# Kernel tuning notes

Measured on AMD Instinct MI355X. Metric: run time of the kernel, lower is better.

## Reference

```python
import jax, jax.numpy as jnp
import numpy as np

DIM = 768
HEADS = 12
HEAD_DIM = DIM // HEADS


def setup_inputs() -> dict:
    key = jax.random.key(0)
    ks = jax.random.split(key, 5)
    s = 0.02
    return {
        "x": jax.random.normal(ks[0], (2, 4096, DIM), dtype=jnp.float32),
        "w_qkv": jax.random.normal(ks[1], (DIM, 3 * DIM), dtype=jnp.float32) * s,
        "b_qkv": jax.random.normal(ks[2], (3 * DIM,), dtype=jnp.float32) * s,
        "w_proj": jax.random.normal(ks[3], (DIM, DIM), dtype=jnp.float32) * s,
        "b_proj": jax.random.normal(ks[4], (DIM,), dtype=jnp.float32) * s,
    }


def reference(x, w_qkv, b_qkv, w_proj, b_proj):
    B, N, _ = x.shape
    scale = HEAD_DIM ** (-0.5)
    qkv = x @ w_qkv + b_qkv                              # [B, N, 3*DIM]
    q, k, v = jnp.split(qkv, 3, axis=-1)
    # 'b n (h d) -> b h n d'
    def to_heads(t):
        return t.reshape(B, N, HEADS, HEAD_DIM).transpose(0, 2, 1, 3)
    q, k, v = to_heads(q), to_heads(k), to_heads(v)
    attn = jnp.einsum('bhnd,bhmd->bhnm', q, k) * scale   # [B, H, N, N]
    attn = jax.nn.softmax(attn, axis=-1)
    out = jnp.einsum('bhnm,bhmd->bhnd', attn, v)         # [B, H, N, D]
    out = out.transpose(0, 2, 1, 3).reshape(B, N, DIM)   # 'b h n d -> b n (h d)'
    return out @ w_proj + b_proj
```

## Files before the change

### kernel.cpp

```cpp
#include <hip/hip_runtime.h>
#include <hip/hip_bf16.h>
#include <stdint.h>

typedef _Float16 f16x8 __attribute__((ext_vector_type(8)));
typedef _Float16 f16x4 __attribute__((ext_vector_type(4)));
typedef uint32_t u32x2 __attribute__((ext_vector_type(2)));
typedef float floatx4 __attribute__((ext_vector_type(4)));

#define NSEQ 4096
#define DIMM 768
#define NHEADS 12
#define HD 64

__device__ __forceinline__ void gload_lds16(const void* g, void* l) {
  typedef __attribute__((address_space(1))) const uint32_t GQ;
  typedef __attribute__((address_space(3))) uint32_t LQ;
  __builtin_amdgcn_global_load_lds((GQ*)g, (LQ*)l, 16, 0, 0);
}

__device__ __forceinline__ uint16_t f16_bits(float v) {
  _Float16 h = (_Float16)v;
  return __builtin_bit_cast(uint16_t, h);
}

__device__ __forceinline__ uint32_t pkrtz(float a, float b) {
  return __builtin_bit_cast(uint32_t, __builtin_amdgcn_cvt_pkrtz(a, b));
}

__device__ __forceinline__ int swz(int row, int e) {
  return row * 64 + ((((e >> 3) ^ (row & 7)) << 3) | (e & 7));
}

__global__ __launch_bounds__(256) void convert_f32_f16(
    const float4* __restrict__ src, f16x8* __restrict__ dst, int n8) {
  const int i = blockIdx.x * 256 + threadIdx.x;
  if (i >= n8) return;
  const float4 a = src[2 * i], b = src[2 * i + 1];
  f16x8 o;
  o[0] = (_Float16)a.x; o[1] = (_Float16)a.y; o[2] = (_Float16)a.z; o[3] = (_Float16)a.w;
  o[4] = (_Float16)b.x; o[5] = (_Float16)b.y; o[6] = (_Float16)b.z; o[7] = (_Float16)b.w;
  dst[i] = o;
}

__global__ __launch_bounds__(256) void transpose_f32_f16(
    const float* __restrict__ src, uint16_t* __restrict__ dst, int R, int C) {
  __shared__ uint16_t tile[32][33];
  const int c0 = blockIdx.x * 32, r0 = blockIdx.y * 32;
  const int tx = threadIdx.x, ty = threadIdx.y;
#pragma unroll
  for (int i = 0; i < 32; i += 8)
    tile[ty + i][tx] = f16_bits(src[(size_t)(r0 + ty + i) * C + (c0 + tx)]);
  __syncthreads();
#pragma unroll
  for (int i = 0; i < 32; i += 8)
    dst[(size_t)(c0 + ty + i) * R + (r0 + tx)] = tile[tx][ty + i];
}

__global__ __launch_bounds__(256) void transpose_b16(
    const uint16_t* __restrict__ src, uint16_t* __restrict__ dst, int R, int C) {
  __shared__ uint16_t tile[32][33];
  const size_t plane = (size_t)blockIdx.z * (size_t)R * (size_t)C;
  const int c0 = blockIdx.x * 32, r0 = blockIdx.y * 32;
  const int tx = threadIdx.x, ty = threadIdx.y;
#pragma unroll
  for (int i = 0; i < 32; i += 8)
    tile[ty + i][tx] = src[plane + (size_t)(r0 + ty + i) * C + (c0 + tx)];
  __syncthreads();
#pragma unroll
  for (int i = 0; i < 32; i += 8)
    dst[plane + (size_t)(c0 + ty + i) * R + (r0 + tx)] = tile[tx][ty + i];
}

__global__ __launch_bounds__(256) void gemm_bt(
    const _Float16* __restrict__ A, const _Float16* __restrict__ Bt,
    const float* __restrict__ bias, int K, int mode,
    void* __restrict__ o0, _Float16* __restrict__ o1, _Float16* __restrict__ o2) {
  __shared__ __attribute__((aligned(16))) _Float16 As[128 * 32];
  __shared__ __attribute__((aligned(16))) _Float16 Bs[128 * 32];
  __shared__ float bias_s[128];
  const int tid = threadIdx.x;
  const int wv = tid >> 6;
  const int lane = tid & 63;
  const int quad = lane >> 4, l16 = lane & 15;
  const int wm = (wv >> 1) * 64, wn = (wv & 1) * 64;
  const int m0 = blockIdx.y * 128, n0 = blockIdx.x * 128;

  if (tid < 128) bias_s[tid] = bias[n0 + tid];

  floatx4 acc[4][4];
#pragma unroll
  for (int i = 0; i < 4; ++i)
#pragma unroll
    for (int j = 0; j < 4; ++j) acc[i][j] = (floatx4){0.f, 0.f, 0.f, 0.f};

  const int ar = tid >> 2, ac = (tid & 3) * 8;
  const _Float16* A0 = A + (size_t)(m0 + ar) * K + ac;
  const _Float16* A1 = A + (size_t)(m0 + 64 + ar) * K + ac;
  const _Float16* B0 = Bt + (size_t)(n0 + ar) * K + ac;
  const _Float16* B1 = Bt + (size_t)(n0 + 64 + ar) * K + ac;

  for (int kt = 0; kt < K; kt += 32) {
    const f16x8 ra0 = *(const f16x8*)(A0 + kt);
    const f16x8 ra1 = *(const f16x8*)(A1 + kt);
    const f16x8 rb0 = *(const f16x8*)(B0 + kt);
    const f16x8 rb1 = *(const f16x8*)(B1 + kt);
    __syncthreads();
    *(f16x8*)&As[tid * 8] = ra0;
    *(f16x8*)&As[2048 + tid * 8] = ra1;
    *(f16x8*)&Bs[tid * 8] = rb0;
    *(f16x8*)&Bs[2048 + tid * 8] = rb1;
    __syncthreads();
    f16x8 af[4], bfr[4];
#pragma unroll
    for (int i = 0; i < 4; ++i)
      af[i] = *(const f16x8*)&As[(wm + i * 16 + l16) * 32 + quad * 8];
#pragma unroll
    for (int j = 0; j < 4; ++j)
      bfr[j] = *(const f16x8*)&Bs[(wn + j * 16 + l16) * 32 + quad * 8];
#pragma unroll
    for (int i = 0; i < 4; ++i)
#pragma unroll
      for (int j = 0; j < 4; ++j)
        acc[i][j] = __builtin_amdgcn_mfma_f32_16x16x32_f16(af[i], bfr[j], acc[i][j], 0, 0, 0);
  }

  if (mode == 0) {
    float* of = (float*)o0;
#pragma unroll
    for (int i = 0; i < 4; ++i)
#pragma unroll
      for (int j = 0; j < 4; ++j) {
        const int col = n0 + wn + j * 16 + l16;
        const float b = bias_s[wn + j * 16 + l16];
        const int mrow = m0 + wm + i * 16 + quad * 4;
#pragma unroll
        for (int r = 0; r < 4; ++r)
          of[(size_t)(mrow + r) * DIMM + col] = acc[i][j][r] + b;
      }
  } else {
    const int sec = n0 / DIMM;
    _Float16* dst = (sec == 0) ? (_Float16*)o0 : (sec == 1) ? o1 : o2;
    const float sc = (sec == 0) ? 0.18033688011112042f : 1.0f;
#pragma unroll
    for (int i = 0; i < 4; ++i)
#pragma unroll
      for (int j = 0; j < 4; ++j) {
        const int n = n0 + wn + j * 16 + l16;
        const int c = n - sec * DIMM;
        const int h = c >> 6, d = c & 63;
        const float b = bias_s[wn + j * 16 + l16];
        const int mrow = m0 + wm + i * 16 + quad * 4;
#pragma unroll
        for (int r = 0; r < 4; ++r) {
          const int m = mrow + r;
          const int bb = m >> 12, nr = m & 4095;
          dst[(((size_t)(bb * NHEADS + h)) * NSEQ + nr) * HD + d] =
              (_Float16)((acc[i][j][r] + b) * sc);
        }
      }
  }
}

__global__ __launch_bounds__(256, 3) void attn(
    const _Float16* __restrict__ Qg, const _Float16* __restrict__ Kg,
    const _Float16* __restrict__ VTg, _Float16* __restrict__ ctx) {
  __shared__ __attribute__((aligned(16))) _Float16 Pt[128 * 64];
  __shared__ __attribute__((aligned(16))) _Float16 Ks[2][64 * 64];
  __shared__ __attribute__((aligned(16))) _Float16 VTs[2][64 * 64];
  const int tid = threadIdx.x;
  const int wv = tid >> 6, lane = tid & 63;
  const int quad = lane >> 4, l16 = lane & 15;
  const int bi = blockIdx.x;
  const int xcd = bi & 7, j = bi >> 3;
  const int bh = xcd * 3 + (j >> 5);
  const int q0 = (j & 31) * 128;
  const int bb = bh / NHEADS, h = bh - bb * NHEADS;
  const _Float16* Qp = Qg + (size_t)bh * NSEQ * HD;
  const _Float16* Kp = Kg + (size_t)bh * NSEQ * HD;
  const _Float16* VTp = VTg + (size_t)bh * HD * NSEQ;

  const int krow = tid >> 3;
  const int kcol = (((tid & 7) ^ ((tid >> 3) & 7)) * 8);
  const int l7 = l16 & 7;

#pragma unroll
  for (int i = 0; i < 4; ++i)
    gload_lds16(Qp + (size_t)(q0 + i * 32 + krow) * HD + kcol, &Pt[(i * 256 + wv * 64) * 8]);
#pragma unroll
  for (int i = 0; i < 2; ++i) {
    gload_lds16(Kp + (size_t)(i * 32 + krow) * HD + kcol, &Ks[0][(i * 256 + wv * 64) * 8]);
    gload_lds16(VTp + (size_t)(i * 32 + krow) * NSEQ + kcol, &VTs[0][(i * 256 + wv * 64) * 8]);
  }
  __syncthreads();

  f16x8 aq[2][2];
#pragma unroll
  for (int it = 0; it < 2; ++it)
#pragma unroll
    for (int ks = 0; ks < 2; ++ks)
      aq[it][ks] = *(const f16x8*)&Pt[swz(wv * 32 + it * 16 + l16, ks * 32 + quad * 8)];

  floatx4 o[2][4];
  float lp[2] = {0.f, 0.f};
#pragma unroll
  for (int it = 0; it < 2; ++it)
#pragma unroll
    for (int jn = 0; jn < 4; ++jn) o[it][jn] = (floatx4){0.f, 0.f, 0.f, 0.f};

  const int prow = wv * 32 + l16;

  auto region = [&](const _Float16* bK, const _Float16* bV, _Float16* wK, _Float16* wV, int kvn) {
    __syncthreads();
#pragma unroll
    for (int i = 0; i < 2; ++i) {
      gload_lds16(Kp + (size_t)(kvn + i * 32 + krow) * HD + kcol, &wK[(i * 256 + wv * 64) * 8]);
      gload_lds16(VTp + (size_t)(i * 32 + krow) * NSEQ + kvn + kcol, &wV[(i * 256 + wv * 64) * 8]);
    }
    floatx4 s[2][4];
#pragma unroll
    for (int it = 0; it < 2; ++it)
#pragma unroll
      for (int im = 0; im < 4; ++im) s[it][im] = (floatx4){0.f, 0.f, 0.f, 0.f};
#pragma unroll
    for (int ks = 0; ks < 2; ++ks) {
#pragma unroll
      for (int im = 0; im < 4; ++im) {
        const f16x8 bk = *(const f16x8*)&bK[swz(im * 16 + l16, ks * 32 + quad * 8)];
        s[0][im] = __builtin_amdgcn_mfma_f32_16x16x32_f16(bk, aq[0][ks], s[0][im], 0, 0, 0);
        s[1][im] = __builtin_amdgcn_mfma_f32_16x16x32_f16(bk, aq[1][ks], s[1][im], 0, 0, 0);
      }
    }
#pragma unroll
    for (int it = 0; it < 2; ++it) {
      const int row = prow + it * 16;
#pragma unroll
      for (int im = 0; im < 4; ++im) {
        float p0 = __builtin_amdgcn_exp2f(s[it][im][0]);
        float p1 = __builtin_amdgcn_exp2f(s[it][im][1]);
        float p2 = __builtin_amdgcn_exp2f(s[it][im][2]);
        float p3 = __builtin_amdgcn_exp2f(s[it][im][3]);
        lp[it] += (p0 + p1) + (p2 + p3);
        const u32x2 packed = {pkrtz(p0, p1), pkrtz(p2, p3)};
        *(f16x4*)&Pt[row * 64 + (((im * 2 + (quad >> 1)) ^ l7) << 3) + (quad & 1) * 4] =
            __builtin_bit_cast(f16x4, packed);
      }
    }
#pragma unroll
    for (int kk = 0; kk < 2; ++kk) {
      const f16x8 ap0 = *(const f16x8*)&Pt[swz(prow, kk * 32 + quad * 8)];
      const f16x8 ap1 = *(const f16x8*)&Pt[swz(prow + 16, kk * 32 + quad * 8)];
#pragma unroll
      for (int jn = 0; jn < 4; ++jn) {
        const f16x8 bv = *(const f16x8*)&bV[swz(jn * 16 + l16, kk * 32 + quad * 8)];
        o[0][jn] = __builtin_amdgcn_mfma_f32_16x16x32_f16(ap0, bv, o[0][jn], 0, 0, 0);
        o[1][jn] = __builtin_amdgcn_mfma_f32_16x16x32_f16(ap1, bv, o[1][jn], 0, 0, 0);
      }
    }
  };

#pragma unroll 1
  for (int p = 0; p < 32; ++p) {
    const int t = 2 * p;
    region(Ks[0], VTs[0], Ks[1], VTs[1], ((t + 1) & 63) * 64);
    region(Ks[1], VTs[1], Ks[0], VTs[0], ((t + 2) & 63) * 64);
  }

#pragma unroll
  for (int it = 0; it < 2; ++it) {
    lp[it] += __shfl_xor(lp[it], 16);
    lp[it] += __shfl_xor(lp[it], 32);
  }
#pragma unroll
  for (int it = 0; it < 2; ++it)
#pragma unroll
    for (int r = 0; r < 4; ++r) {
      const int q = q0 + wv * 32 + it * 16 + quad * 4 + r;
      const float lq = __shfl(lp[it], (lane & 48) | (quad * 4 + r));
      const float inv = 1.0f / lq;
      _Float16* dst = ctx + (size_t)(bb * NSEQ + q) * DIMM + h * HD;
#pragma unroll
      for (int jn = 0; jn < 4; ++jn)
        dst[jn * 16 + l16] = (_Float16)(o[it][jn][r] * inv);
    }
}

extern "C" void kernel_launch(void* const* d_in, const int* in_sizes, int n_in,
                              void* d_out, int out_size, void* d_ws, size_t ws_size,
                              hipStream_t stream) {
  char* ws = (char*)d_ws;
  _Float16* xc = (_Float16*)ws;      ws += (size_t)8192 * 768 * 2;
  _Float16* wqkvT = (_Float16*)ws;   ws += (size_t)2304 * 768 * 2;
  _Float16* wprojT = (_Float16*)ws;  ws += (size_t)768 * 768 * 2;
  const size_t qkv_elems = (size_t)2 * NHEADS * NSEQ * HD;
  _Float16* Qb = (_Float16*)ws;      ws += qkv_elems * 2;
  _Float16* Kb = (_Float16*)ws;      ws += qkv_elems * 2;
  _Float16* Vb = (_Float16*)ws;      ws += qkv_elems * 2;
  _Float16* VTb = (_Float16*)ws;     ws += qkv_elems * 2;
  _Float16* ctx = xc;

  const dim3 tb(32, 8, 1);
  const dim3 b256(256, 1, 1);
  hipLaunchKernelGGL(convert_f32_f16, dim3(3072, 1, 1), b256, 0, stream,
                     (const float4*)d_in[0], (f16x8*)xc, 8192 * 768 / 8);
  hipLaunchKernelGGL(transpose_f32_f16, dim3(72, 24, 1), tb, 0, stream,
                     (const float*)d_in[1], (uint16_t*)wqkvT, 768, 2304);
  hipLaunchKernelGGL(transpose_f32_f16, dim3(24, 24, 1), tb, 0, stream,
                     (const float*)d_in[3], (uint16_t*)wprojT, 768, 768);
  hipLaunchKernelGGL(gemm_bt, dim3(18, 64, 1), b256, 0, stream,
                     xc, wqkvT, (const float*)d_in[2], 768, 1, (void*)Qb, Kb, Vb);
  hipLaunchKernelGGL(transpose_b16, dim3(2, 128, 24), tb, 0, stream,
                     (const uint16_t*)Vb, (uint16_t*)VTb, 4096, 64);
  hipLaunchKernelGGL(attn, dim3(768, 1, 1), b256, 0, stream, Qb, Kb, VTb, ctx);
  hipLaunchKernelGGL(gemm_bt, dim3(6, 64, 1), b256, 0, stream,
                     ctx, wprojT, (const float*)d_in[4], 768, 0, d_out,
                     (_Float16*)nullptr, (_Float16*)nullptr);
}
```

Baseline: 300.9 us.

## Split attention KV across waves, keep P in registers, reduce partial outputs in LDS

The attention kernel now gives each block 64 queries, and each wave handles a different 16-key slice of every 64-key KV tile. Probabilities stay in registers and feed a 16x16x16 MFMA directly, so the LDS round trip for P is gone. Partial outputs and row sums from the four waves are combined through LDS at the end, and the grid doubles to 1536 blocks. This removes P staging and some per-region syncs but adds a cross-wave reduction and reloads each K/V tile for half as many queries. The final redundant prefetch is also skipped.

```diff
diff --git a/kernel.cpp b/kernel.cpp
--- a/kernel.cpp
+++ b/kernel.cpp
@@ -164,16 +164,15 @@
 __global__ __launch_bounds__(256, 3) void attn(
     const _Float16* __restrict__ Qg, const _Float16* __restrict__ Kg,
     const _Float16* __restrict__ VTg, _Float16* __restrict__ ctx) {
-  __shared__ __attribute__((aligned(16))) _Float16 Pt[128 * 64];
-  __shared__ __attribute__((aligned(16))) _Float16 Ks[2][64 * 64];
-  __shared__ __attribute__((aligned(16))) _Float16 VTs[2][64 * 64];
+  __shared__ __attribute__((aligned(16))) _Float16 KV[4][64 * 64];
+  __shared__ float l_arr[256];
   const int tid = threadIdx.x;
   const int wv = tid >> 6, lane = tid & 63;
   const int quad = lane >> 4, l16 = lane & 15;
   const int bi = blockIdx.x;
   const int xcd = bi & 7, j = bi >> 3;
-  const int bh = xcd * 3 + (j >> 5);
-  const int q0 = (j & 31) * 128;
+  const int bh = xcd * 3 + (j >> 6);
+  const int q0 = (j & 63) * 64;
   const int bb = bh / NHEADS, h = bh - bb * NHEADS;
   const _Float16* Qp = Qg + (size_t)bh * NSEQ * HD;
   const _Float16* Kp = Kg + (size_t)bh * NSEQ * HD;
@@ -181,107 +180,127 @@
 
   const int krow = tid >> 3;
   const int kcol = (((tid & 7) ^ ((tid >> 3) & 7)) * 8);
-  const int l7 = l16 & 7;
-
-#pragma unroll
-  for (int i = 0; i < 4; ++i)
-    gload_lds16(Qp + (size_t)(q0 + i * 32 + krow) * HD + kcol, &Pt[(i * 256 + wv * 64) * 8]);
+
+  f16x8 aq[4][2];
+#pragma unroll
+  for (int qn = 0; qn < 4; ++qn)
+#pragma unroll
+    for (int ks = 0; ks < 2; ++ks)
+      aq[qn][ks] = *(const f16x8*)(Qp + (size_t)(q0 + qn * 16 + l16) * HD + ks * 32 + quad * 8);
+
 #pragma unroll
   for (int i = 0; i < 2; ++i) {
-    gload_lds16(Kp + (size_t)(i * 32 + krow) * HD + kcol, &Ks[0][(i * 256 + wv * 64) * 8]);
-    gload_lds16(VTp + (size_t)(i * 32 + krow) * NSEQ + kcol, &VTs[0][(i * 256 + wv * 64) * 8]);
-  }
-  __syncthreads();
-
-  f16x8 aq[2][2];
-#pragma unroll
-  for (int it = 0; it < 2; ++it)
-#pragma unroll
-    for (int ks = 0; ks < 2; ++ks)
-      aq[it][ks] = *(const f16x8*)&Pt[swz(wv * 32 + it * 16 + l16, ks * 32 + quad * 8)];
-
-  floatx4 o[2][4];
-  float lp[2] = {0.f, 0.f};
-#pragma unroll
-  for (int it = 0; it < 2; ++it)
-#pragma unroll
-    for (int jn = 0; jn < 4; ++jn) o[it][jn] = (floatx4){0.f, 0.f, 0.f, 0.f};
-
-  const int prow = wv * 32 + l16;
-
-  auto region = [&](const _Float16* bK, const _Float16* bV, _Float16* wK, _Float16* wV, int kvn) {
+    gload_lds16(Kp + (size_t)(i * 32 + krow) * HD + kcol, &KV[0][(i * 256 + wv * 64) * 8]);
+    gload_lds16(VTp + (size_t)(i * 32 + krow) * NSEQ + kcol, &KV[2][(i * 256 + wv * 64) * 8]);
+  }
+
+  floatx4 o[4][4];
+  float lpp[4] = {0.f, 0.f, 0.f, 0.f};
+#pragma unroll
+  for (int qn = 0; qn < 4; ++qn)
+#pragma unroll
+    for (int jn = 0; jn < 4; ++jn) o[qn][jn] = (floatx4){0.f, 0.f, 0.f, 0.f};
+
+  auto region = [&](const _Float16* bK, const _Float16* bV, _Float16* wK, _Float16* wV,
+                    int kvn, bool prefetch) {
     __syncthreads();
-#pragma unroll
-    for (int i = 0; i < 2; ++i) {
-      gload_lds16(Kp + (size_t)(kvn + i * 32 + krow) * HD + kcol, &wK[(i * 256 + wv * 64) * 8]);
-      gload_lds16(VTp + (size_t)(i * 32 + krow) * NSEQ + kvn + kcol, &wV[(i * 256 + wv * 64) * 8]);
-    }
-    floatx4 s[2][4];
-#pragma unroll
-    for (int it = 0; it < 2; ++it)
-#pragma unroll
-      for (int im = 0; im < 4; ++im) s[it][im] = (floatx4){0.f, 0.f, 0.f, 0.f};
-#pragma unroll
-    for (int ks = 0; ks < 2; ++ks) {
-#pragma unroll
-      for (int im = 0; im < 4; ++im) {
-        const f16x8 bk = *(const f16x8*)&bK[swz(im * 16 + l16, ks * 32 + quad * 8)];
-        s[0][im] = __builtin_amdgcn_mfma_f32_16x16x32_f16(bk, aq[0][ks], s[0][im], 0, 0, 0);
-        s[1][im] = __builtin_amdgcn_mfma_f32_16x16x32_f16(bk, aq[1][ks], s[1][im], 0, 0, 0);
+    if (prefetch) {
+#pragma unroll
+      for (int i = 0; i < 2; ++i) {
+        gload_lds16(Kp + (size_t)(kvn + i * 32 + krow) * HD + kcol, &wK[(i * 256 + wv * 64) * 8]);
+        gload_lds16(VTp + (size_t)(i * 32 + krow) * NSEQ + kvn + kcol, &wV[(i * 256 + wv * 64) * 8]);
       }
     }
-#pragma unroll
-    for (int it = 0; it < 2; ++it) {
-      const int row = prow + it * 16;
-#pragma unroll
-      for (int im = 0; im < 4; ++im) {
-        float p0 = __builtin_amdgcn_exp2f(s[it][im][0]);
-        float p1 = __builtin_amdgcn_exp2f(s[it][im][1]);
-        float p2 = __builtin_amdgcn_exp2f(s[it][im][2]);
-        float p3 = __builtin_amdgcn_exp2f(s[it][im][3]);
-        lp[it] += (p0 + p1) + (p2 + p3);
-        const u32x2 packed = {pkrtz(p0, p1), pkrtz(p2, p3)};
-        *(f16x4*)&Pt[row * 64 + (((im * 2 + (quad >> 1)) ^ l7) << 3) + (quad & 1) * 4] =
-            __builtin_bit_cast(f16x4, packed);
-      }
-    }
-#pragma unroll
-    for (int kk = 0; kk < 2; ++kk) {
-      const f16x8 ap0 = *(const f16x8*)&Pt[swz(prow, kk * 32 + quad * 8)];
-      const f16x8 ap1 = *(const f16x8*)&Pt[swz(prow + 16, kk * 32 + quad * 8)];
-#pragma unroll
-      for (int jn = 0; jn < 4; ++jn) {
-        const f16x8 bv = *(const f16x8*)&bV[swz(jn * 16 + l16, kk * 32 + quad * 8)];
-        o[0][jn] = __builtin_amdgcn_mfma_f32_16x16x32_f16(ap0, bv, o[0][jn], 0, 0, 0);
-        o[1][jn] = __builtin_amdgcn_mfma_f32_16x16x32_f16(ap1, bv, o[1][jn], 0, 0, 0);
-      }
-    }
+    const f16x8 bk0 = *(const f16x8*)&bK[swz(wv * 16 + l16, quad * 8)];
+    const f16x8 bk1 = *(const f16x8*)&bK[swz(wv * 16 + l16, 32 + quad * 8)];
+    floatx4 s[4];
+#pragma unroll
+    for (int qn = 0; qn < 4; ++qn) {
+      s[qn] = __builtin_amdgcn_mfma_f32_16x16x32_f16(bk0, aq[qn][0],
+                                                     (floatx4){0.f, 0.f, 0.f, 0.f}, 0, 0, 0);
+      s[qn] = __builtin_amdgcn_mfma_f32_16x16x32_f16(bk1, aq[qn][1], s[qn], 0, 0, 0);
+    }
+    f16x4 ap[4];
+#pragma unroll
+    for (int qn = 0; qn < 4; ++qn) {
+      const float p0 = __builtin_amdgcn_exp2f(s[qn][0]);
+      const float p1 = __builtin_amdgcn_exp2f(s[qn][1]);
+      const float p2 = __builtin_amdgcn_exp2f(s[qn][2]);
+      const float p3 = __builtin_amdgcn_exp2f(s[qn][3]);
+      lpp[qn] += (p0 + p1) + (p2 + p3);
+      const u32x2 pk = {pkrtz(p0, p1), pkrtz(p2, p3)};
+      ap[qn] = __builtin_bit_cast(f16x4, pk);
+    }
+    f16x4 bv[4];
+#pragma unroll
+    for (int jn = 0; jn < 4; ++jn) {
+      const int row = jn * 16 + l16;
+      bv[jn] = *(const f16x4*)&bV[row * 64 + (((wv * 2 + (quad >> 1)) ^ (row & 7)) << 3) +
+                                  (quad & 1) * 4];
+    }
+#pragma unroll
+    for (int qn = 0; qn < 4; ++qn)
+#pragma unroll
+      for (int jn = 0; jn < 4; ++jn)
+        o[qn][jn] = __builtin_amdgcn_mfma_f32_16x16x16f16(ap[qn], bv[jn], o[qn][jn], 0, 0, 0);
   };
 
 #pragma unroll 1
   for (int p = 0; p < 32; ++p) {
     const int t = 2 * p;
-    region(Ks[0], VTs[0], Ks[1], VTs[1], ((t + 1) & 63) * 64);
-    region(Ks[1], VTs[1], Ks[0], VTs[0], ((t + 2) & 63) * 64);
-  }
-
-#pragma unroll
-  for (int it = 0; it < 2; ++it) {
-    lp[it] += __shfl_xor(lp[it], 16);
-    lp[it] += __shfl_xor(lp[it], 32);
-  }
-#pragma unroll
-  for (int it = 0; it < 2; ++it)
-#pragma unroll
-    for (int r = 0; r < 4; ++r) {
-      const int q = q0 + wv * 32 + it * 16 + quad * 4 + r;
-      const float lq = __shfl(lp[it], (lane & 48) | (quad * 4 + r));
-      const float inv = 1.0f / lq;
-      _Float16* dst = ctx + (size_t)(bb * NSEQ + q) * DIMM + h * HD;
+    region(KV[0], KV[2], KV[1], KV[3], ((t + 1) & 63) * 64, true);
+    region(KV[1], KV[3], KV[0], KV[2], ((t + 2) & 63) * 64, p < 31);
+  }
+
+#pragma unroll
+  for (int qn = 0; qn < 4; ++qn) {
+    lpp[qn] += __shfl_xor(lpp[qn], 16);
+    lpp[qn] += __shfl_xor(lpp[qn], 32);
+  }
+  __syncthreads();
+  if (quad == 0) {
+#pragma unroll
+    for (int qn = 0; qn < 4; ++qn) l_arr[wv * 64 + qn * 16 + l16] = lpp[qn];
+  }
+  {
+    _Float16* Op = KV[wv];
+#pragma unroll
+    for (int qn = 0; qn < 4; ++qn)
 #pragma unroll
       for (int jn = 0; jn < 4; ++jn)
-        dst[jn * 16 + l16] = (_Float16)(o[it][jn][r] * inv);
-    }
+#pragma unroll
+        for (int r = 0; r < 4; ++r)
+          Op[swz(qn * 16 + quad * 4 + r, jn * 16 + l16)] = (_Float16)o[qn][jn][r];
+  }
+  __syncthreads();
+  {
+    const int rrow = wv * 16 + (lane >> 2);
+    const int c0 = (lane & 3) * 16;
+    const float l_row = l_arr[rrow] + l_arr[64 + rrow] + l_arr[128 + rrow] + l_arr[192 + rrow];
+    const float inv = 1.0f / l_row;
+    float accv[16];
+#pragma unroll
+    for (int k = 0; k < 16; ++k) accv[k] = 0.f;
+#pragma unroll
+    for (int w = 0; w < 4; ++w) {
+      const f16x8 pa = *(const f16x8*)&KV[w][swz(rrow, c0)];
+      const f16x8 pb = *(const f16x8*)&KV[w][swz(rrow, c0 + 8)];
+#pragma unroll
+      for (int k = 0; k < 8; ++k) {
+        accv[k] += (float)pa[k];
+        accv[8 + k] += (float)pb[k];
+      }
+    }
+    f16x8 oa, ob;
+#pragma unroll
+    for (int k = 0; k < 8; ++k) {
+      oa[k] = (_Float16)(accv[k] * inv);
+      ob[k] = (_Float16)(accv[8 + k] * inv);
+    }
+    _Float16* dst = ctx + (size_t)(bb * NSEQ + q0 + rrow) * DIMM + h * HD + c0;
+    *(f16x8*)dst = oa;
+    *(f16x8*)(dst + 8) = ob;
+  }
 }
 
 extern "C" void kernel_launch(void* const* d_in, const int* in_sizes, int n_in,
@@ -310,7 +329,7 @@
                      xc, wqkvT, (const float*)d_in[2], 768, 1, (void*)Qb, Kb, Vb);
   hipLaunchKernelGGL(transpose_b16, dim3(2, 128, 24), tb, 0, stream,
                      (const uint16_t*)Vb, (uint16_t*)VTb, 4096, 64);
-  hipLaunchKernelGGL(attn, dim3(768, 1, 1), b256, 0, stream, Qb, Kb, VTb, ctx);
+  hipLaunchKernelGGL(attn, dim3(1536, 1, 1), b256, 0, stream, Qb, Kb, VTb, ctx);
   hipLaunchKernelGGL(gemm_bt, dim3(6, 64, 1), b256, 0, stream,
                      ctx, wprojT, (const float*)d_in[4], 768, 0, d_out,
                      (_Float16*)nullptr, (_Float16*)nullptr);
```

After: 311.9 us. 3.6% more time.
